# Performance work log

Measured on AMD Instinct MI355X. Metric: run time of the kernel, lower is better.

Reference implementation:

```python
import jax, jax.numpy as jnp
import numpy as np

D_MODEL = 2048
N_HEADS = 16
HEAD_DIM = D_MODEL // N_HEADS
D_FF = ((int(8 * D_MODEL / 3) + 64) // 64) * 64  # 5504
B, T = 2, 2048
EPS = 1e-8
NEG = -1e9


def rotate_half(x):
    half = x.shape[-1] // 2
    return jnp.concatenate([-x[..., half:], x[..., :half]], axis=-1)


def apply_rope(x, cos, sin):
    # x: [B,H,T,hd]; cos/sin: [T,hd] -> [1,1,T,hd]
    c = cos[None, None, :, :]
    s = sin[None, None, :, :]
    return x * c + rotate_half(x) * s


def rmsnorm(x, w):
    rms = jnp.sqrt(jnp.mean(x * x, axis=-1, keepdims=True))
    return w * x / (rms + EPS)


def setup_inputs() -> dict:
    key = jax.random.key(0)
    ks = jax.random.split(key, 12)
    x = jax.random.normal(ks[0], (B, T, D_MODEL), dtype=jnp.float32)
    # RoPE tables
    inv_freq = 1.0 / (10000.0 ** (jnp.arange(0, HEAD_DIM, 2, dtype=jnp.float32) / HEAD_DIM))
    pos = jnp.arange(T, dtype=jnp.float32)
    freqs = pos[:, None] * inv_freq[None, :]          # [T, hd/2]
    emb = jnp.concatenate([freqs, freqs], axis=-1)    # [T, hd]
    cos, sin = jnp.cos(emb), jnp.sin(emb)
    # causal additive mask [T,T]
    mask = jnp.where(jnp.tril(jnp.ones((T, T), dtype=bool)), 0.0, NEG).astype(jnp.float32)
    scale = 0.02
    Wq = jax.random.normal(ks[1], (D_MODEL, D_MODEL), dtype=jnp.float32) * scale
    Wk = jax.random.normal(ks[2], (D_MODEL, D_MODEL), dtype=jnp.float32) * scale
    Wv = jax.random.normal(ks[3], (D_MODEL, D_MODEL), dtype=jnp.float32) * scale
    Wo = jax.random.normal(ks[4], (D_MODEL, D_MODEL), dtype=jnp.float32) * scale
    W1 = jax.random.normal(ks[5], (D_FF, D_MODEL), dtype=jnp.float32) * scale
    W2 = jax.random.normal(ks[6], (D_FF, D_MODEL), dtype=jnp.float32) * scale
    Wout = jax.random.normal(ks[7], (D_MODEL, D_FF), dtype=jnp.float32) * scale
    g1 = jnp.ones((D_MODEL,), dtype=jnp.float32)
    g2 = jnp.ones((D_MODEL,), dtype=jnp.float32)
    return {"x": x, "cos": cos, "sin": sin, "mask": mask,
            "g1": g1, "g2": g2, "Wq": Wq, "Wk": Wk, "Wv": Wv, "Wo": Wo,
            "W1": W1, "W2": W2, "Wout": Wout}


def reference(x, cos, sin, mask, g1, g2, Wq, Wk, Wv, Wo, W1, W2, Wout):
    Bb, Tt, Dd = x.shape

    def split_heads(t):  # [B,T,D] -> [B,H,T,hd]
        return t.reshape(Bb, Tt, N_HEADS, HEAD_DIM).transpose(0, 2, 1, 3)

    h = rmsnorm(x, g1)
    Q = apply_rope(split_heads(h @ Wq.T), cos, sin)
    K = apply_rope(split_heads(h @ Wk.T), cos, sin)
    V = split_heads(h @ Wv.T)
    scores = jnp.einsum('bhqd,bhkd->bhqk', Q, K) / jnp.sqrt(jnp.float32(HEAD_DIM))
    scores = scores + mask  # broadcast [T,T] over [B,H,T,T]
    weights = jax.nn.softmax(scores, axis=-1)
    attn = jnp.einsum('bhqk,bhkd->bhqd', weights, V)
    attn = attn.transpose(0, 2, 1, 3).reshape(Bb, Tt, Dd)
    x = x + attn @ Wo.T

    h2 = rmsnorm(x, g2)
    ff = (jax.nn.silu(h2 @ W1.T) * (h2 @ W2.T)) @ Wout.T
    return x + ff
```

## Files before the change

kernel.cpp:

```cpp
#include <hip/hip_runtime.h>


using bf16 = __bf16;
typedef __bf16 bf16x2 __attribute__((ext_vector_type(2)));
typedef __bf16 bf16x8 __attribute__((ext_vector_type(8)));
typedef float f32x4 __attribute__((ext_vector_type(4)));

#define MFMA_BF16(a, b, c) __builtin_amdgcn_mfma_f32_16x16x32_bf16((a), (b), (c), 0, 0, 0)

__device__ __forceinline__ void gld_lds16(const void* g, void* l) {
  __builtin_amdgcn_global_load_lds((const __attribute__((address_space(1))) void*)g,
                                   (__attribute__((address_space(3))) void*)l,
                                   16, 0, 0);
}

__global__ void detect_dtype(const unsigned int* __restrict__ X, int* __restrict__ flag) {
  const int tid = threadIdx.x;
  const unsigned int w = X[tid];
  const unsigned int e_lo = (w >> 7) & 0xFF;
  const unsigned int e_hi = (w >> 23) & 0xFF;
  const bool sane = (e_lo >= 97u && e_lo <= 157u) && (e_hi >= 97u && e_hi <= 157u);
  const unsigned long long m = __ballot(sane);
  if (tid == 0) *flag = (__popcll(m) > 48) ? 1 : 0;
}

__global__ __launch_bounds__(256) void convert_in(const void* __restrict__ src,
                                                  bf16* __restrict__ dst,
                                                  const int* __restrict__ flag) {
  const size_t i = ((size_t)blockIdx.x * 256 + threadIdx.x) * 8;
  if (*flag) {
    *(bf16x8*)(dst + i) = *(const bf16x8*)((const bf16*)src + i);
  } else {
    const float* s = (const float*)src;
    float4 a = *(const float4*)(s + i);
    float4 b = *(const float4*)(s + i + 4);
    bf16x8 o;
    o[0] = (bf16)a.x; o[1] = (bf16)a.y; o[2] = (bf16)a.z; o[3] = (bf16)a.w;
    o[4] = (bf16)b.x; o[5] = (bf16)b.y; o[6] = (bf16)b.z; o[7] = (bf16)b.w;
    *(bf16x8*)(dst + i) = o;
  }
}

__global__ __launch_bounds__(256) void rmsnorm_bf16(const bf16* __restrict__ X,
                                                    const bf16* __restrict__ g,
                                                    bf16* __restrict__ Hout) {
  const int row = blockIdx.x, tid = threadIdx.x;
  const size_t off = (size_t)row * 2048 + tid * 8;
  bf16x8 x8 = *(const bf16x8*)(X + off);
  float v[8];
  float s = 0.f;
#pragma unroll
  for (int j = 0; j < 8; ++j) { v[j] = (float)x8[j]; s += v[j] * v[j]; }
#pragma unroll
  for (int o = 32; o; o >>= 1) s += __shfl_xor(s, o);
  __shared__ float red[4];
  if ((tid & 63) == 0) red[tid >> 6] = s;
  __syncthreads();
  const float tot = red[0] + red[1] + red[2] + red[3];
  const float inv = 1.f / (sqrtf(tot * (1.f / 2048.f)) + 1e-8f);
  bf16x8 g8 = *(const bf16x8*)(g + tid * 8);
  bf16x8 o8;
#pragma unroll
  for (int j = 0; j < 8; ++j) o8[j] = (bf16)((float)g8[j] * v[j] * inv);
  *(bf16x8*)(Hout + off) = o8;
}

__global__ __launch_bounds__(256) void rmsnorm_f32(const float* __restrict__ X,
                                                   const bf16* __restrict__ g,
                                                   bf16* __restrict__ Hout) {
  const int row = blockIdx.x, tid = threadIdx.x;
  const size_t off = (size_t)row * 2048 + tid * 8;
  float4 a0 = *(const float4*)(X + off);
  float4 a1 = *(const float4*)(X + off + 4);
  float v[8] = {a0.x, a0.y, a0.z, a0.w, a1.x, a1.y, a1.z, a1.w};
  float s = 0.f;
#pragma unroll
  for (int j = 0; j < 8; ++j) s += v[j] * v[j];
#pragma unroll
  for (int o = 32; o; o >>= 1) s += __shfl_xor(s, o);
  __shared__ float red[4];
  if ((tid & 63) == 0) red[tid >> 6] = s;
  __syncthreads();
  const float tot = red[0] + red[1] + red[2] + red[3];
  const float inv = 1.f / (sqrtf(tot * (1.f / 2048.f)) + 1e-8f);
  bf16x8 g8 = *(const bf16x8*)(g + tid * 8);
  bf16x8 o8;
#pragma unroll
  for (int j = 0; j < 8; ++j) o8[j] = (bf16)((float)g8[j] * v[j] * inv);
  *(bf16x8*)(Hout + off) = o8;
}

__global__ __launch_bounds__(256) void rope_k(bf16* __restrict__ Q, bf16* __restrict__ Kg,
                                              const bf16* __restrict__ cosb,
                                              const bf16* __restrict__ sinb) {
  const int tid = threadIdx.x;
  const int rr = tid >> 7;
  const int c = tid & 127;
  const int bt = blockIdx.x * 2 + rr;
  const int t = bt & 2047;
  const int h = c >> 3;
  const int d0 = (c & 7) * 8;
  const size_t row = (size_t)bt * 2048;
  const int i0 = h * 128 + d0;
  bf16x8 c0 = *(const bf16x8*)(cosb + t * 128 + d0);
  bf16x8 c1 = *(const bf16x8*)(cosb + t * 128 + d0 + 64);
  bf16x8 s0 = *(const bf16x8*)(sinb + t * 128 + d0);
  bf16x8 s1 = *(const bf16x8*)(sinb + t * 128 + d0 + 64);
  bf16x8 qa = *(const bf16x8*)(Q + row + i0);
  bf16x8 qb = *(const bf16x8*)(Q + row + i0 + 64);
  bf16x8 ka = *(const bf16x8*)(Kg + row + i0);
  bf16x8 kb = *(const bf16x8*)(Kg + row + i0 + 64);
  bf16x8 qo0, qo1, ko0, ko1;
#pragma unroll
  for (int j = 0; j < 8; ++j) {
    float cj0 = (float)c0[j], cj1 = (float)c1[j];
    float sj0 = (float)s0[j], sj1 = (float)s1[j];
    float qaj = (float)qa[j], qbj = (float)qb[j];
    float kaj = (float)ka[j], kbj = (float)kb[j];
    qo0[j] = (bf16)(qaj * cj0 - qbj * sj0);
    qo1[j] = (bf16)(qbj * cj1 + qaj * sj1);
    ko0[j] = (bf16)(kaj * cj0 - kbj * sj0);
    ko1[j] = (bf16)(kbj * cj1 + kaj * sj1);
  }
  *(bf16x8*)(Q + row + i0) = qo0;
  *(bf16x8*)(Q + row + i0 + 64) = qo1;
  *(bf16x8*)(Kg + row + i0) = ko0;
  *(bf16x8*)(Kg + row + i0 + 64) = ko1;
}

template <int EPI>
__global__ __launch_bounds__(256) void gemm_bt(const bf16* __restrict__ A,
                                               const bf16* __restrict__ W,
                                               bf16* __restrict__ Cb, float* __restrict__ Cf,
                                               const bf16* __restrict__ resb,
                                               const float* __restrict__ resf,
                                               const bf16* __restrict__ mulb,
                                               const int* __restrict__ oflag,
                                               int M, int N, int K) {
  __shared__ bf16 As[2][128 * 32];
  __shared__ bf16 Ws[2][128 * 32];
  const int tid = threadIdx.x;
  const int wave = tid >> 6, lane = tid & 63;
  const int quad = lane >> 4, l15 = lane & 15;
  const int wm = wave >> 1, wn = wave & 1;
  const int m0 = blockIdx.y * 128, n0 = blockIdx.x * 128;

  f32x4 acc[4][4];
#pragma unroll
  for (int i = 0; i < 4; ++i)
#pragma unroll
    for (int j = 0; j < 4; ++j) acc[i][j] = {0.f, 0.f, 0.f, 0.f};

  const int srow = lane >> 2;
  const int skk = (lane & 3) * 8;
  const bf16* Ab = A + (size_t)m0 * K;
  const bf16* Wb = W + (size_t)n0 * K;

  auto stage = [&](int buf, int kb) {
    const int k0 = kb << 5;
#pragma unroll
    for (int c = 0; c < 2; ++c) {
      const int r = (wave * 2 + c) * 16 + srow;
      gld_lds16(Ab + (size_t)r * K + k0 + skk, (char*)As[buf] + (wave * 2 + c) * 1024);
      gld_lds16(Wb + (size_t)r * K + k0 + skk, (char*)Ws[buf] + (wave * 2 + c) * 1024);
    }
  };
  auto compute = [&](int buf) {
    bf16x8 af[4], wf[4];
#pragma unroll
    for (int mt = 0; mt < 4; ++mt)
      af[mt] = *(const bf16x8*)&As[buf][(wm * 64 + mt * 16 + l15) * 32 + quad * 8];
#pragma unroll
    for (int nt = 0; nt < 4; ++nt)
      wf[nt] = *(const bf16x8*)&Ws[buf][(wn * 64 + nt * 16 + l15) * 32 + quad * 8];
#pragma unroll
    for (int mt = 0; mt < 4; ++mt)
#pragma unroll
      for (int nt = 0; nt < 4; ++nt)
        acc[mt][nt] = MFMA_BF16(af[mt], wf[nt], acc[mt][nt]);
  };

  const int nk = K >> 5;
  stage(0, 0);
  for (int kb = 0; kb < nk; kb += 2) {
    __syncthreads();
    if (kb + 1 < nk) stage(1, kb + 1);
    compute(0);
    __syncthreads();
    if (kb + 2 < nk) stage(0, kb + 2);
    compute(1);
  }

  const int obf = (EPI == 4 && oflag) ? *oflag : 0;
#pragma unroll
  for (int mt = 0; mt < 4; ++mt) {
#pragma unroll
    for (int nt = 0; nt < 4; ++nt) {
#pragma unroll
      for (int r = 0; r < 4; ++r) {
        const int row = m0 + wm * 64 + mt * 16 + quad * 4 + r;
        const int col = n0 + wn * 64 + nt * 16 + l15;
        const size_t idx = (size_t)row * N + col;
        const float v = acc[mt][nt][r];
        if constexpr (EPI == 0) {
          Cb[idx] = (bf16)v;
        } else if constexpr (EPI == 1) {
          Cf[idx] = v + (float)resb[idx];
        } else if constexpr (EPI == 2) {
          Cb[idx] = (bf16)(v / (1.f + __expf(-v)));
        } else if constexpr (EPI == 3) {
          Cb[idx] = (bf16)((float)mulb[idx] * v);
        } else {
          const float rres = resf[idx] + v;
          if (obf) Cb[idx] = (bf16)rres;
          else     Cf[idx] = rres;
        }
      }
    }
  }
}

__global__ __launch_bounds__(256) void flash_attn(const bf16* __restrict__ Q,
                                                  const bf16* __restrict__ Kg,
                                                  const bf16* __restrict__ Vg,
                                                  bf16* __restrict__ O) {
  __shared__ bf16 Ks[2][64 * 128];
  __shared__ bf16 Vt[128 * 64];
  __shared__ bf16 Ps[4 * 16 * 64];
  const int tid = threadIdx.x;
  const int wave = tid >> 6, lane = tid & 63;
  const int quad = lane >> 4, l15 = lane & 15;
  const int bh = blockIdx.x;
  const int b = bh >> 4, h = bh & 15;
  const size_t base = (size_t)b * 2048 * 2048 + h * 128;
  const float scale = 0.08838834764831845f;

  bf16x8 vva[2], vvb[2];

  auto stageK = [&](int buf, int kb) {
    const int k0 = kb * 64;
#pragma unroll
    for (int c = 0; c < 4; ++c) {
      const int ch = tid + 256 * c;
      const int row = ch >> 4;
      const int scb = ((ch & 15) * 16) ^ ((row & 7) << 4);
      gld_lds16((const char*)(Kg + base + (size_t)(k0 + row) * 2048) + scb,
                (char*)Ks[buf] + wave * 1024 + c * 4096);
    }
  };
  auto loadV = [&](int kb) {
    const int k0 = kb * 64;
#pragma unroll
    for (int c = 0; c < 2; ++c) {
      const int tau = tid + 256 * c;
      const int kp = tau & 31;
      const int d0 = (tau >> 5) * 8;
      vva[c] = *(const bf16x8*)(Vg + base + (size_t)(k0 + 2 * kp) * 2048 + d0);
      vvb[c] = *(const bf16x8*)(Vg + base + (size_t)(k0 + 2 * kp + 1) * 2048 + d0);
    }
  };
  auto writeV = [&]() {
#pragma unroll
    for (int c = 0; c < 2; ++c) {
      const int tau = tid + 256 * c;
      const int kp = tau & 31;
      const int d0 = (tau >> 5) * 8;
#pragma unroll
      for (int j = 0; j < 8; ++j) {
        bf16x2 pr = {vva[c][j], vvb[c][j]};
        const int d = d0 + j;
        *(bf16x2*)((char*)Vt + d * 128 + ((4 * kp) ^ ((d & 7) << 4))) = pr;
      }
    }
  };

#pragma unroll 1
  for (int half = 0; half < 2; ++half) {
    const int qt = half ? (31 - (int)blockIdx.y) : (int)blockIdx.y;
    const int q0 = qt * 64;

    bf16x8 qf[4];
    {
      const bf16* qrow = Q + base + (size_t)(q0 + wave * 16 + l15) * 2048;
#pragma unroll
      for (int ks = 0; ks < 4; ++ks) qf[ks] = *(const bf16x8*)(qrow + ks * 32 + quad * 8);
    }

    f32x4 o[8];
#pragma unroll
    for (int i = 0; i < 8; ++i) o[i] = {0.f, 0.f, 0.f, 0.f};
    float m_r[4] = {-1e30f, -1e30f, -1e30f, -1e30f};
    float l_r[4] = {0.f, 0.f, 0.f, 0.f};

    loadV(0);
    stageK(0, 0);
    if (qt >= 1) stageK(1, 1);
    asm volatile("s_waitcnt vmcnt(4)" ::: "memory");
    __builtin_amdgcn_s_barrier();
    __builtin_amdgcn_sched_barrier(0);

#pragma unroll 1
    for (int kb = 0; kb <= qt; ++kb) {
      const int cur = kb & 1;
      const int k0 = kb * 64;

      writeV();
      if (kb + 1 <= qt) loadV(kb + 1);

      f32x4 s[4];
      __builtin_amdgcn_s_setprio(1);
#pragma unroll
      for (int nt = 0; nt < 4; ++nt) {
        s[nt] = {0.f, 0.f, 0.f, 0.f};
        const int krow = nt * 16 + l15;
#pragma unroll
        for (int ks = 0; ks < 4; ++ks) {
          bf16x8 kf = *(const bf16x8*)((char*)Ks[cur] + krow * 256 +
                                       ((ks * 64 + quad * 16) ^ ((krow & 7) << 4)));
          s[nt] = MFMA_BF16(qf[ks], kf, s[nt]);
        }
      }
      __builtin_amdgcn_s_setprio(0);

      float sv[4][4];
#pragma unroll
      for (int nt = 0; nt < 4; ++nt) {
#pragma unroll
        for (int r = 0; r < 4; ++r) {
          float v = s[nt][r] * scale;
          const int key = k0 + nt * 16 + l15;
          const int qq = q0 + wave * 16 + quad * 4 + r;
          if (key > qq) v = -1e9f;
          sv[nt][r] = v;
        }
      }

#pragma unroll
      for (int r = 0; r < 4; ++r) {
        float rmax = fmaxf(fmaxf(sv[0][r], sv[1][r]), fmaxf(sv[2][r], sv[3][r]));
#pragma unroll
        for (int off = 1; off < 16; off <<= 1) rmax = fmaxf(rmax, __shfl_xor(rmax, off));
        const float mnew = fmaxf(m_r[r], rmax);
        const float alpha = __expf(m_r[r] - mnew);
        float psum = 0.f;
        const int qrow = quad * 4 + r;
#pragma unroll
        for (int nt = 0; nt < 4; ++nt) {
          const float p = __expf(sv[nt][r] - mnew);
          psum += p;
          *(bf16*)((char*)Ps + wave * 2048 + qrow * 128 +
                   ((2 * (nt * 16 + l15)) ^ ((qrow & 7) << 4))) = (bf16)p;
        }
#pragma unroll
        for (int off = 1; off < 16; off <<= 1) psum += __shfl_xor(psum, off);
        l_r[r] = l_r[r] * alpha + psum;
        m_r[r] = mnew;
#pragma unroll
        for (int nt2 = 0; nt2 < 8; ++nt2) o[nt2][r] *= alpha;
      }

      asm volatile("s_waitcnt lgkmcnt(0)" ::: "memory");
      __builtin_amdgcn_s_barrier();
      __builtin_amdgcn_sched_barrier(0);

      if (kb + 2 <= qt) stageK(cur, kb + 2);

      __builtin_amdgcn_s_setprio(1);
#pragma unroll
      for (int ks2 = 0; ks2 < 2; ++ks2) {
        bf16x8 pf = *(const bf16x8*)((char*)Ps + wave * 2048 + l15 * 128 +
                                     ((ks2 * 64 + quad * 16) ^ ((l15 & 7) << 4)));
#pragma unroll
        for (int nt2 = 0; nt2 < 8; ++nt2) {
          const int drow = nt2 * 16 + l15;
          bf16x8 vf = *(const bf16x8*)((char*)Vt + drow * 128 +
                                       ((ks2 * 64 + quad * 16) ^ ((drow & 7) << 4)));
          o[nt2] = MFMA_BF16(pf, vf, o[nt2]);
        }
      }
      __builtin_amdgcn_s_setprio(0);

      asm volatile("s_waitcnt lgkmcnt(0)" ::: "memory");
      asm volatile("s_waitcnt vmcnt(8)" ::: "memory");
      __builtin_amdgcn_s_barrier();
      __builtin_amdgcn_sched_barrier(0);
    }

#pragma unroll
    for (int nt2 = 0; nt2 < 8; ++nt2) {
#pragma unroll
      for (int r = 0; r < 4; ++r) {
        const int qq = q0 + wave * 16 + quad * 4 + r;
        const int dd = nt2 * 16 + l15;
        O[base + (size_t)qq * 2048 + dd] = (bf16)(o[nt2][r] / l_r[r]);
      }
    }
  }
}

extern "C" void kernel_launch(void* const* d_in, const int* in_sizes, int n_in,
                              void* d_out, int out_size, void* d_ws, size_t ws_size,
                              hipStream_t stream) {
  const void* x_raw = d_in[0];
  const void* cos_raw = d_in[1];
  const void* sin_raw = d_in[2];
  const void* g1_raw = d_in[4];
  const void* g2_raw = d_in[5];
  const void* W_raw[7] = {d_in[6], d_in[7], d_in[8], d_in[9], d_in[10], d_in[11], d_in[12]};

  char* ws = (char*)d_ws;
  const size_t MB = 1048576ull;
  int* flag = (int*)ws;
  bf16* g1c = (bf16*)(ws + 4096);
  bf16* g2c = (bf16*)(ws + 12288);
  bf16* cosc = (bf16*)(ws + 65536);
  bf16* sinc = (bf16*)(ws + 655360);
  bf16* xc   = (bf16*)(ws + 2 * MB);
  bf16* wslot= (bf16*)(ws + 18 * MB);
  bf16* hbuf = (bf16*)(ws + 41 * MB);
  bf16* qbuf = (bf16*)(ws + 57 * MB);
  bf16* kbuf = (bf16*)(ws + 73 * MB);
  bf16* vbuf = (bf16*)(ws + 89 * MB);
  bf16* abuf = (bf16*)(ws + 105 * MB);
  float* x1  = (float*)(ws + 57 * MB);
  bf16* h2   = (bf16*)(ws + 41 * MB);
  bf16* ubuf = (bf16*)(ws + 89 * MB);

  const int M = 4096;
  dim3 blk(256);

  detect_dtype<<<1, 64, 0, stream>>>((const unsigned int*)x_raw, flag);

  convert_in<<<4096, blk, 0, stream>>>(x_raw, xc, flag);
  convert_in<<<128, blk, 0, stream>>>(cos_raw, cosc, flag);
  convert_in<<<128, blk, 0, stream>>>(sin_raw, sinc, flag);
  convert_in<<<1, blk, 0, stream>>>(g1_raw, g1c, flag);
  convert_in<<<1, blk, 0, stream>>>(g2_raw, g2c, flag);

  rmsnorm_bf16<<<M, blk, 0, stream>>>(xc, g1c, hbuf);

  convert_in<<<2048, blk, 0, stream>>>(W_raw[0], wslot, flag);
  gemm_bt<0><<<dim3(16, 32), blk, 0, stream>>>(hbuf, wslot, qbuf, nullptr, nullptr, nullptr, nullptr, nullptr, M, 2048, 2048);
  convert_in<<<2048, blk, 0, stream>>>(W_raw[1], wslot, flag);
  gemm_bt<0><<<dim3(16, 32), blk, 0, stream>>>(hbuf, wslot, kbuf, nullptr, nullptr, nullptr, nullptr, nullptr, M, 2048, 2048);
  convert_in<<<2048, blk, 0, stream>>>(W_raw[2], wslot, flag);
  gemm_bt<0><<<dim3(16, 32), blk, 0, stream>>>(hbuf, wslot, vbuf, nullptr, nullptr, nullptr, nullptr, nullptr, M, 2048, 2048);

  rope_k<<<M / 2, blk, 0, stream>>>(qbuf, kbuf, cosc, sinc);
  flash_attn<<<dim3(32, 16), blk, 0, stream>>>(qbuf, kbuf, vbuf, abuf);

  convert_in<<<2048, blk, 0, stream>>>(W_raw[3], wslot, flag);
  gemm_bt<1><<<dim3(16, 32), blk, 0, stream>>>(abuf, wslot, nullptr, x1, xc, nullptr, nullptr, nullptr, M, 2048, 2048);

  rmsnorm_f32<<<M, blk, 0, stream>>>(x1, g2c, h2);

  convert_in<<<5504, blk, 0, stream>>>(W_raw[4], wslot, flag);
  gemm_bt<2><<<dim3(43, 32), blk, 0, stream>>>(h2, wslot, ubuf, nullptr, nullptr, nullptr, nullptr, nullptr, M, 5504, 2048);
  convert_in<<<5504, blk, 0, stream>>>(W_raw[5], wslot, flag);
  gemm_bt<3><<<dim3(43, 32), blk, 0, stream>>>(h2, wslot, ubuf, nullptr, nullptr, nullptr, ubuf, nullptr, M, 5504, 2048);
  convert_in<<<5504, blk, 0, stream>>>(W_raw[6], wslot, flag);
  gemm_bt<4><<<dim3(16, 32), blk, 0, stream>>>(ubuf, wslot, (bf16*)d_out, (float*)d_out, nullptr, x1, nullptr, flag, M, 2048, 5504);
}
```

Measured before the change: 991.4 us.

## Triple-buffer GEMM LDS staging with vmcnt waits and MFMA-fragment layout

Moves the bf16 GEMM main loop from double to triple buffering in LDS. It issues global-to-LDS loads two K-steps ahead and waits with an explicit vmcnt count, so only one barrier is needed per step instead of two. The staging layout changes so each 16-row group is stored in the order the MFMA fragments read it, letting each lane fetch its fragment as one contiguous 16-byte load. It also raises wave priority around the MFMA block. LDS use grows by half, which may reduce occupancy, and the hand-written vmcnt(4) wait assumes exactly four loads are outstanding per stage.

```diff
diff --git a/kernel.cpp b/kernel.cpp
--- a/kernel.cpp
+++ b/kernel.cpp
@@ -137,8 +137,8 @@
                                                const bf16* __restrict__ mulb,
                                                const int* __restrict__ oflag,
                                                int M, int N, int K) {
-  __shared__ bf16 As[2][128 * 32];
-  __shared__ bf16 Ws[2][128 * 32];
+  __shared__ bf16 As[3][128 * 32];
+  __shared__ bf16 Ws[3][128 * 32];
   const int tid = threadIdx.x;
   const int wave = tid >> 6, lane = tid & 63;
   const int quad = lane >> 4, l15 = lane & 15;
@@ -151,45 +151,54 @@
 #pragma unroll
     for (int j = 0; j < 4; ++j) acc[i][j] = {0.f, 0.f, 0.f, 0.f};
 
-  const int srow = lane >> 2;
-  const int skk = (lane & 3) * 8;
   const bf16* Ab = A + (size_t)m0 * K;
   const bf16* Wb = W + (size_t)n0 * K;
+  const int sr = lane & 15;
+  const int sc = (lane >> 4) * 8;
 
   auto stage = [&](int buf, int kb) {
     const int k0 = kb << 5;
 #pragma unroll
     for (int c = 0; c < 2; ++c) {
-      const int r = (wave * 2 + c) * 16 + srow;
-      gld_lds16(Ab + (size_t)r * K + k0 + skk, (char*)As[buf] + (wave * 2 + c) * 1024);
-      gld_lds16(Wb + (size_t)r * K + k0 + skk, (char*)Ws[buf] + (wave * 2 + c) * 1024);
+      const int g = wave * 2 + c;
+      gld_lds16(Ab + (size_t)(g * 16 + sr) * K + k0 + sc, (char*)As[buf] + g * 1024);
+      gld_lds16(Wb + (size_t)(g * 16 + sr) * K + k0 + sc, (char*)Ws[buf] + g * 1024);
     }
   };
   auto compute = [&](int buf) {
     bf16x8 af[4], wf[4];
 #pragma unroll
     for (int mt = 0; mt < 4; ++mt)
-      af[mt] = *(const bf16x8*)&As[buf][(wm * 64 + mt * 16 + l15) * 32 + quad * 8];
+      af[mt] = *(const bf16x8*)((const char*)As[buf] + (wm * 4 + mt) * 1024 + lane * 16);
 #pragma unroll
     for (int nt = 0; nt < 4; ++nt)
-      wf[nt] = *(const bf16x8*)&Ws[buf][(wn * 64 + nt * 16 + l15) * 32 + quad * 8];
+      wf[nt] = *(const bf16x8*)((const char*)Ws[buf] + (wn * 4 + nt) * 1024 + lane * 16);
+    __builtin_amdgcn_s_setprio(1);
 #pragma unroll
     for (int mt = 0; mt < 4; ++mt)
 #pragma unroll
       for (int nt = 0; nt < 4; ++nt)
         acc[mt][nt] = MFMA_BF16(af[mt], wf[nt], acc[mt][nt]);
+    __builtin_amdgcn_s_setprio(0);
   };
 
   const int nk = K >> 5;
   stage(0, 0);
-  for (int kb = 0; kb < nk; kb += 2) {
-    __syncthreads();
-    if (kb + 1 < nk) stage(1, kb + 1);
-    compute(0);
-    __syncthreads();
-    if (kb + 2 < nk) stage(0, kb + 2);
-    compute(1);
+  stage(1, 1);
+  int bc = 0, bn2 = 2;
+  for (int kb = 0; kb < nk - 1; ++kb) {
+    asm volatile("s_waitcnt vmcnt(4)" ::: "memory");
+    __builtin_amdgcn_s_barrier();
+    __builtin_amdgcn_sched_barrier(0);
+    if (kb + 2 < nk) stage(bn2, kb + 2);
+    compute(bc);
+    bc = (bc == 2) ? 0 : bc + 1;
+    bn2 = (bn2 == 2) ? 0 : bn2 + 1;
   }
+  asm volatile("s_waitcnt vmcnt(0)" ::: "memory");
+  __builtin_amdgcn_s_barrier();
+  __builtin_amdgcn_sched_barrier(0);
+  compute(bc);
 
   const int obf = (EPI == 4 && oflag) ? *oflag : 0;
 #pragma unroll
```

Measured after the change: 1.215 ms. +22.5%, slower.
